# Performance work log

Measured on AMD Instinct MI355X. Metric: run time of the kernel, lower is better.

The kernel has to match this reference:

```python
import jax, jax.numpy as jnp
import numpy as np

N, C, E = 50000, 128, 600000


def setup_inputs() -> dict:
    key = jax.random.key(0)
    ks = jax.random.split(key, 10)
    s = 1.0 / np.sqrt(C)
    x = jax.random.normal(ks[0], (N, C), jnp.float32)
    edge_index = jax.random.randint(ks[1], (2, E), 0, N)
    edge_weight = jax.random.uniform(ks[2], (E,), jnp.float32)
    # learned params
    p_score = jax.random.normal(ks[3], (C,), jnp.float32) * s      # TopKPooling projection
    W0 = jax.random.normal(ks[4], (C, C), jnp.float32) * s         # initial GCN weight
    w_ih = jax.random.normal(ks[5], (3 * C, C), jnp.float32) * s   # GRU input weights (r,z,n)
    w_hh = jax.random.normal(ks[6], (3 * C, C), jnp.float32) * s   # GRU hidden weights
    b_ih = jnp.zeros((3 * C,), jnp.float32)
    b_hh = jnp.zeros((3 * C,), jnp.float32)
    w_lin = jax.random.normal(ks[7], (1, C), jnp.float32) * s      # head Linear(C,1)
    b_lin = jnp.zeros((1,), jnp.float32)
    return dict(x=x, edge_index=edge_index, edge_weight=edge_weight,
                p_score=p_score, W0=W0, w_ih=w_ih, w_hh=w_hh,
                b_ih=b_ih, b_hh=b_hh, w_lin=w_lin, b_lin=b_lin)


def _evolve_gcnh(x, edge_index, edge_weight, p_score, W0, w_ih, w_hh, b_ih, b_hh):
    n, c = x.shape
    # --- TopKPooling: score = tanh((x.p)/||p||), keep top k=C nodes, scale by score
    score = jnp.tanh((x @ p_score) / jnp.linalg.norm(p_score))
    vals, perm = jax.lax.top_k(score, c)           # tanh monotone -> same perm as raw score
    x_tilde = x[perm] * vals[:, None]              # [C, C]
    # --- GRU single step: batch = C rows of the weight matrix, hidden = W0
    gi = x_tilde @ w_ih.T + b_ih                   # [C, 3C]
    gh = W0 @ w_hh.T + b_hh                        # [C, 3C]
    i_r, i_z, i_n = jnp.split(gi, 3, axis=1)
    h_r, h_z, h_n = jnp.split(gh, 3, axis=1)
    r = jax.nn.sigmoid(i_r + h_r)
    z = jax.nn.sigmoid(i_z + h_z)
    ng = jnp.tanh(i_n + r * h_n)
    W = (1.0 - z) * ng + z * W0                    # evolved GCN weight [C, C]
    # --- GCNConv with fixed W: gcn_norm with self loops, then scatter-sum
    loops = jnp.arange(n)
    row = jnp.concatenate([edge_index[0], loops])  # source
    col = jnp.concatenate([edge_index[1], loops])  # target
    w = jnp.concatenate([edge_weight, jnp.ones((n,), edge_weight.dtype)])
    deg = jax.ops.segment_sum(w, col, num_segments=n)
    dis = jnp.where(deg > 0, jax.lax.rsqrt(jnp.where(deg > 0, deg, 1.0)), 0.0)
    norm = dis[row] * w * dis[col]                 # [E+N]
    xw = x @ W                                     # [N, C]
    out = jax.ops.segment_sum(norm[:, None] * xw[row], col, num_segments=n)
    return out


def reference(x, edge_index, edge_weight, p_score, W0, w_ih, w_hh, b_ih, b_hh, w_lin, b_lin):
    h = _evolve_gcnh(x, edge_index, edge_weight, p_score, W0, w_ih, w_hh, b_ih, b_hh)
    h = jax.nn.relu(h)
    return h @ w_lin.T + b_lin                     # [N, 1]
```

## Files before the change

### kernel.cpp

```cpp
#include <hip/hip_runtime.h>
#include <stdint.h>

#define C 128
#define RSTRIDE 64

typedef __attribute__((ext_vector_type(8))) short short8;
typedef __attribute__((ext_vector_type(4))) float f32x4;

__device__ __forceinline__ unsigned f32_orderable(float f) {
  unsigned u = __float_as_uint(f);
  return (u & 0x80000000u) ? ~u : (u | 0x80000000u);
}
__device__ __forceinline__ unsigned short f32_to_bf16_rn(float f) {
  unsigned u = __float_as_uint(f);
  unsigned rounding = 0x7FFFu + ((u >> 16) & 1u);
  return (unsigned short)((u + rounding) >> 16);
}
__device__ __forceinline__ float bf16_to_f32(unsigned short h) {
  return __uint_as_float(((unsigned)h) << 16);
}

__global__ __launch_bounds__(256) void k_score(const float* __restrict__ x,
                                               const float* __restrict__ p,
                                               float* __restrict__ score,
                                               unsigned* __restrict__ hist, int N) {
  int l = threadIdx.x & 63;
  int n = blockIdx.x * 4 + (threadIdx.x >> 6);
  if (n >= N) return;
  float2 xv = ((const float2*)(x + (size_t)n * C))[l];
  float2 pv = ((const float2*)p)[l];
  float s = xv.x * pv.x + xv.y * pv.y;
  for (int o = 32; o > 0; o >>= 1) s += __shfl_down(s, o, 64);
  if (l == 0) {
    score[n] = s;
    atomicAdd(&hist[f32_orderable(s) >> 16], 1u);
  }
}

__global__ __launch_bounds__(256) void k_fill(const int* __restrict__ ei,
                                              const float* __restrict__ ew,
                                              int* __restrict__ cnt,
                                              unsigned* __restrict__ csr, int E) {
  int base = (blockIdx.x * 256 + threadIdx.x) * 4;
  if (base >= E) return;
  if (base + 3 < E) {
    int4   s4 = *(const int4*)(ei + base);
    int4   d4 = *(const int4*)(ei + E + base);
    float4 w4 = *(const float4*)(ew + base);
    int r0 = atomicAdd(&cnt[d4.x], 1);
    int r1 = atomicAdd(&cnt[d4.y], 1);
    int r2 = atomicAdd(&cnt[d4.z], 1);
    int r3 = atomicAdd(&cnt[d4.w], 1);
    if (r0 > RSTRIDE - 1) r0 = RSTRIDE - 1;
    if (r1 > RSTRIDE - 1) r1 = RSTRIDE - 1;
    if (r2 > RSTRIDE - 1) r2 = RSTRIDE - 1;
    if (r3 > RSTRIDE - 1) r3 = RSTRIDE - 1;
    csr[((size_t)d4.x << 6) + r0] = ((unsigned)f32_to_bf16_rn(w4.x) << 16) | (unsigned)s4.x;
    csr[((size_t)d4.y << 6) + r1] = ((unsigned)f32_to_bf16_rn(w4.y) << 16) | (unsigned)s4.y;
    csr[((size_t)d4.z << 6) + r2] = ((unsigned)f32_to_bf16_rn(w4.z) << 16) | (unsigned)s4.z;
    csr[((size_t)d4.w << 6) + r3] = ((unsigned)f32_to_bf16_rn(w4.w) << 16) | (unsigned)s4.w;
  } else {
    for (int e = base; e < E; ++e) {
      int src = ei[e];
      int dst = ei[E + e];
      int r = atomicAdd(&cnt[dst], 1);
      if (r > RSTRIDE - 1) r = RSTRIDE - 1;
      csr[((size_t)dst << 6) + r] = ((unsigned)f32_to_bf16_rn(ew[e]) << 16) | (unsigned)src;
    }
  }
}

__global__ __launch_bounds__(1024) void k_topk_rowdeg(const unsigned* __restrict__ hist,
                                                      const float* __restrict__ score,
                                                      const float* __restrict__ p,
                                                      int* __restrict__ perm,
                                                      float* __restrict__ vals, int N,
                                                      const unsigned* __restrict__ csr,
                                                      const int* __restrict__ cnt,
                                                      float* __restrict__ dis) {
  int t = threadIdx.x;
  if (blockIdx.x == 0) {
    __shared__ unsigned csum[1024];
    __shared__ uint64_t keys[1024];
    __shared__ int tcs;
    __shared__ unsigned Ts, cnt_sh;
    __shared__ float s_inv;
    if (t < 64) {
      float2 v = ((const float2*)p)[t];
      float s = v.x * v.x + v.y * v.y;
      for (int o = 32; o > 0; o >>= 1) s += __shfl_down(s, o, 64);
      if (t == 0) s_inv = 1.0f / sqrtf(s);
    }
    if (t == 0) cnt_sh = 0;
    unsigned s = 0;
    const unsigned* hb = hist + t * 64;
    for (int b = 0; b < 64; ++b) s += hb[b];
    csum[t] = s;
    __syncthreads();
    for (int off = 1; off < 1024; off <<= 1) {
      unsigned v = (t + off < 1024) ? csum[t + off] : 0u;
      __syncthreads();
      csum[t] += v;
      __syncthreads();
    }
    unsigned St  = csum[t];
    unsigned St1 = (t < 1023) ? csum[t + 1] : 0u;
    if (St >= 128u && St1 < 128u) tcs = t;
    __syncthreads();
    if (t == 0) {
      int tc = tcs;
      unsigned cum = (tc < 1023) ? csum[tc + 1] : 0u;
      unsigned T = (unsigned)(tc * 64);
      for (int b = tc * 64 + 63; b >= tc * 64; --b) {
        cum += hist[b];
        if (cum >= 128u) { T = (unsigned)b; break; }
      }
      Ts = T;
    }
    __syncthreads();
    unsigned T = Ts;
    for (int k = t; k < N; k += 1024) {
      unsigned u = f32_orderable(score[k]);
      if ((u >> 16) >= T) {
        unsigned pos = atomicAdd(&cnt_sh, 1u);
        if (pos < 1024u) keys[pos] = ((uint64_t)u << 32) | (unsigned)(~k);
      }
    }
    __syncthreads();
    unsigned M = cnt_sh;
    if (M > 1024u) M = 1024u;
    if (t >= (int)M) keys[t] = 0ull;
    __syncthreads();
    for (int size = 2; size <= 1024; size <<= 1) {
      for (int stride = size >> 1; stride > 0; stride >>= 1) {
        int pr = t ^ stride;
        if (pr > t) {
          uint64_t a = keys[t], b = keys[pr];
          bool desc = ((t & size) == 0);
          if (desc ? (a < b) : (a > b)) { keys[t] = b; keys[pr] = a; }
        }
        __syncthreads();
      }
    }
    if (t < C) {
      uint64_t key = keys[t];
      unsigned n = ~(unsigned)(key & 0xFFFFFFFFull);
      unsigned u = (unsigned)(key >> 32);
      unsigned bbits = (u & 0x80000000u) ? (u & 0x7FFFFFFFu) : ~u;
      float sc = __uint_as_float(bbits);
      perm[t] = (int)n;
      vals[t] = tanhf(sc * s_inv);
    }
  } else {
    int n = (blockIdx.x - 1) * 128 + (t >> 3);
    if (n >= N) return;
    int l = t & 7;
    int c = cnt[n];
    if (c > RSTRIDE) c = RSTRIDE;
    const unsigned* row = csr + ((size_t)n << 6);
    float s = 0.0f;
    for (int i = l; i < c; i += 8) s += bf16_to_f32((unsigned short)(row[i] >> 16));
    for (int o = 4; o > 0; o >>= 1) s += __shfl_down(s, o, 8);
    if (l == 0) dis[n] = rsqrtf(1.0f + s);
  }
}

__global__ __launch_bounds__(128) void k_gru(const float* __restrict__ x,
                                             const int* __restrict__ perm,
                                             const float* __restrict__ vals,
                                             const float* __restrict__ W0,
                                             const float* __restrict__ w_ih,
                                             const float* __restrict__ w_hh,
                                             const float* __restrict__ b_ih,
                                             const float* __restrict__ b_hh,
                                             float* __restrict__ W) {
  __shared__ float xt[C], h0[C];
  int i = blockIdx.x, j = threadIdx.x;
  xt[j] = x[(size_t)perm[i] * C + j] * vals[i];
  h0[j] = W0[i * C + j];
  __syncthreads();
  float ir = b_ih[j], iz = b_ih[C + j], in_ = b_ih[2 * C + j];
  float hr = b_hh[j], hz = b_hh[C + j], hn  = b_hh[2 * C + j];
  const float4* wr = (const float4*)(w_ih + (size_t)j * C);
  const float4* wz = (const float4*)(w_ih + (size_t)(C + j) * C);
  const float4* wn = (const float4*)(w_ih + (size_t)(2 * C + j) * C);
  const float4* vr = (const float4*)(w_hh + (size_t)j * C);
  const float4* vz = (const float4*)(w_hh + (size_t)(C + j) * C);
  const float4* vn = (const float4*)(w_hh + (size_t)(2 * C + j) * C);
  const float4* xt4 = (const float4*)xt;
  const float4* h04 = (const float4*)h0;
  for (int k = 0; k < C / 4; ++k) {
    float4 xv = xt4[k], hv = h04[k], a;
    a = wr[k]; ir  += xv.x * a.x + xv.y * a.y + xv.z * a.z + xv.w * a.w;
    a = wz[k]; iz  += xv.x * a.x + xv.y * a.y + xv.z * a.z + xv.w * a.w;
    a = wn[k]; in_ += xv.x * a.x + xv.y * a.y + xv.z * a.z + xv.w * a.w;
    a = vr[k]; hr  += hv.x * a.x + hv.y * a.y + hv.z * a.z + hv.w * a.w;
    a = vz[k]; hz  += hv.x * a.x + hv.y * a.y + hv.z * a.z + hv.w * a.w;
    a = vn[k]; hn  += hv.x * a.x + hv.y * a.y + hv.z * a.z + hv.w * a.w;
  }
  float r  = 1.0f / (1.0f + expf(-(ir + hr)));
  float z  = 1.0f / (1.0f + expf(-(iz + hz)));
  float ng = tanhf(in_ + r * hn);
  W[i * C + j] = (1.0f - z) * ng + z * h0[j];
}

__global__ __launch_bounds__(256) void k_wsplit(const float* __restrict__ W,
                                                unsigned short* __restrict__ Bhi,
                                                unsigned short* __restrict__ Blo) {
  int gtid = blockIdx.x * 256 + threadIdx.x;
  int tile = gtid >> 6;
  int l = gtid & 63;
  int ct = tile >> 2, kt = tile & 3;
  int j = ct * 16 + (l & 15);
  int kbase = kt * 32 + (l >> 4) * 8;
  size_t o = (size_t)(tile * 64 + l) * 8;
#pragma unroll
  for (int e = 0; e < 8; ++e) {
    float w = W[(size_t)(kbase + e) * C + j];
    unsigned short hi = f32_to_bf16_rn(w);
    float rem = w - bf16_to_f32(hi);
    Bhi[o + e] = hi;
    Blo[o + e] = f32_to_bf16_rn(rem);
  }
}

__global__ __launch_bounds__(256) void k_xw(const float* __restrict__ x,
                                            const unsigned short* __restrict__ Bhi,
                                            const unsigned short* __restrict__ Blo,
                                            unsigned short* __restrict__ xwh, int N) {
  int wid = threadIdx.x >> 6;
  int l = threadIdx.x & 63;
  int rt = blockIdx.x * 4 + wid;
  int r0 = rt * 16;
  if (r0 >= N) return;
  int row16 = l & 15;
  int kgrp = l >> 4;

  short8 ahi[4], alo[4];
#pragma unroll
  for (int kt = 0; kt < 4; ++kt) {
    int r = r0 + row16;
    if (r >= N) r = N - 1;
    const float* xp = x + (size_t)r * C + kt * 32 + kgrp * 8;
    float4 a0 = *(const float4*)xp;
    float4 a1 = *(const float4*)(xp + 4);
    float v[8] = {a0.x, a0.y, a0.z, a0.w, a1.x, a1.y, a1.z, a1.w};
#pragma unroll
    for (int e = 0; e < 8; ++e) {
      unsigned short hi = f32_to_bf16_rn(v[e]);
      float rem = v[e] - bf16_to_f32(hi);
      ahi[kt][e] = (short)hi;
      alo[kt][e] = (short)f32_to_bf16_rn(rem);
    }
  }

  f32x4 acc[8];
#pragma unroll
  for (int ct = 0; ct < 8; ++ct) acc[ct] = (f32x4){0.f, 0.f, 0.f, 0.f};

#pragma unroll
  for (int ct = 0; ct < 8; ++ct) {
#pragma unroll
    for (int kt = 0; kt < 4; ++kt) {
      const short8 bhi = *(const short8*)(Bhi + (size_t)((ct * 4 + kt) * 64 + l) * 8);
      const short8 blo = *(const short8*)(Blo + (size_t)((ct * 4 + kt) * 64 + l) * 8);
      acc[ct] = __builtin_amdgcn_mfma_f32_16x16x32_bf16(ahi[kt], bhi, acc[ct], 0, 0, 0);
      acc[ct] = __builtin_amdgcn_mfma_f32_16x16x32_bf16(alo[kt], bhi, acc[ct], 0, 0, 0);
      acc[ct] = __builtin_amdgcn_mfma_f32_16x16x32_bf16(ahi[kt], blo, acc[ct], 0, 0, 0);
      acc[ct] = __builtin_amdgcn_mfma_f32_16x16x32_bf16(alo[kt], blo, acc[ct], 0, 0, 0);
    }
  }

#pragma unroll
  for (int ct = 0; ct < 8; ++ct) {
    int col = ct * 16 + row16;
#pragma unroll
    for (int reg = 0; reg < 4; ++reg) {
      int row = r0 + kgrp * 4 + reg;
      if (row < N) xwh[(size_t)row * C + col] = f32_to_bf16_rn(acc[ct][reg]);
    }
  }
}

__device__ __forceinline__ float4 bf16x4_to_f32(uint2 pk) {
  float4 r;
  r.x = __uint_as_float(pk.x << 16);
  r.y = __uint_as_float(pk.x & 0xFFFF0000u);
  r.z = __uint_as_float(pk.y << 16);
  r.w = __uint_as_float(pk.y & 0xFFFF0000u);
  return r;
}
__global__ __launch_bounds__(256) void k_gather_final(const unsigned* __restrict__ csr,
                                                      const int* __restrict__ cnt,
                                                      const unsigned short* __restrict__ xwh,
                                                      const float* __restrict__ dis,
                                                      const float* __restrict__ w_lin,
                                                      const float* __restrict__ b_lin,
                                                      float* __restrict__ out, int N) {
  int tid = threadIdx.x;
  int n = blockIdx.x * 8 + (tid >> 5);
  if (n >= N) return;
  int l = tid & 31;
  const unsigned* row = csr + ((size_t)n << 6);
  int c = cnt[n];
  if (c > RSTRIDE) c = RSTRIDE;
  float4 acc = make_float4(0.f, 0.f, 0.f, 0.f);

  unsigned ent[16];
#pragma unroll
  for (int i = 0; i < 16; ++i) ent[i] = row[i];
#pragma unroll
  for (int i = 0; i < 16; ++i) {
    int si = ent[i] & 0xFFFF;
    float wi = (i < c) ? bf16_to_f32((unsigned short)(ent[i] >> 16)) * dis[si] : 0.0f;
    uint2 pk = ((const uint2*)(xwh + (size_t)si * C))[l];
    float4 v = bf16x4_to_f32(pk);
    acc.x += wi * v.x;
    acc.y += wi * v.y;
    acc.z += wi * v.z;
    acc.w += wi * v.w;
  }
  for (int i = 16; i < c; ++i) {
    unsigned e0 = row[i];
    int s0 = e0 & 0xFFFF;
    float w0 = bf16_to_f32((unsigned short)(e0 >> 16)) * dis[s0];
    uint2 pk = ((const uint2*)(xwh + (size_t)s0 * C))[l];
    float4 v = bf16x4_to_f32(pk);
    acc.x += w0 * v.x;
    acc.y += w0 * v.y;
    acc.z += w0 * v.z;
    acc.w += w0 * v.w;
  }
  float dn = dis[n];
  uint2 ps = ((const uint2*)(xwh + (size_t)n * C))[l];
  float4 xv = bf16x4_to_f32(ps);
  acc.x = fmaf(dn, xv.x, acc.x) * dn;
  acc.y = fmaf(dn, xv.y, acc.y) * dn;
  acc.z = fmaf(dn, xv.z, acc.z) * dn;
  acc.w = fmaf(dn, xv.w, acc.w) * dn;
  float4 wl = ((const float4*)w_lin)[l];
  float psum = fmaxf(acc.x, 0.f) * wl.x + fmaxf(acc.y, 0.f) * wl.y
             + fmaxf(acc.z, 0.f) * wl.z + fmaxf(acc.w, 0.f) * wl.w;
  for (int o = 16; o > 0; o >>= 1) psum += __shfl_down(psum, o, 32);
  if (l == 0) out[n] = psum + b_lin[0];
}

extern "C" void kernel_launch(void* const* d_in, const int* in_sizes, int n_in,
                              void* d_out, int out_size, void* d_ws, size_t ws_size,
                              hipStream_t stream) {
  const float* x     = (const float*)d_in[0];
  const int*   ei    = (const int*)d_in[1];
  const float* ew    = (const float*)d_in[2];
  const float* p     = (const float*)d_in[3];
  const float* W0    = (const float*)d_in[4];
  const float* w_ih  = (const float*)d_in[5];
  const float* w_hh  = (const float*)d_in[6];
  const float* b_ih  = (const float*)d_in[7];
  const float* b_hh  = (const float*)d_in[8];
  const float* w_lin = (const float*)d_in[9];
  const float* b_lin = (const float*)d_in[10];
  int N = in_sizes[0] / C;
  int E = in_sizes[2];

  char* ws = (char*)d_ws;
  size_t off = 0;
  auto alloc = [&](size_t bytes) -> void* {
    void* q = ws + off;
    off = (off + bytes + 255) & ~(size_t)255;
    return q;
  };
  unsigned short* xwh = (unsigned short*)alloc((size_t)N * C * 2);
  unsigned* csr    = (unsigned*)alloc((size_t)N * RSTRIDE * 4);
  float*    score  = (float*)alloc((size_t)N * 4);
  float*    dis    = (float*)alloc((size_t)N * 4);
  size_t zstart = off;
  unsigned* hist   = (unsigned*)alloc(65536 * 4);
  int*      cnt    = (int*)alloc((size_t)N * 4);
  size_t zend = off;
  int*      perm   = (int*)alloc(C * 4);
  float*    vals   = (float*)alloc(C * 4);
  float*    W      = (float*)alloc(C * C * 4);
  unsigned short* Bhi = (unsigned short*)alloc(C * C * 2);
  unsigned short* Blo = (unsigned short*)alloc(C * C * 2);

  hipMemsetAsync(ws + zstart, 0, zend - zstart, stream);

  k_score<<<(N + 3) / 4, 256, 0, stream>>>(x, p, score, hist, N);
  k_fill<<<(E / 4 + 255) / 256, 256, 0, stream>>>(ei, ew, cnt, csr, E);
  int RB = (N + 127) / 128;
  k_topk_rowdeg<<<1 + RB, 1024, 0, stream>>>(hist, score, p, perm, vals, N, csr, cnt, dis);
  k_gru<<<C, C, 0, stream>>>(x, perm, vals, W0, w_ih, w_hh, b_ih, b_hh, W);
  k_wsplit<<<8, 256, 0, stream>>>(W, Bhi, Blo);
  {
    int rowtiles = (N + 15) / 16;
    int blocks = (rowtiles + 3) / 4;
    k_xw<<<blocks, 256, 0, stream>>>(x, Bhi, Blo, xwh, N);
  }
  k_gather_final<<<(N + 7) / 8, 256, 0, stream>>>(csr, cnt, xwh, dis,
                                                  w_lin, b_lin, (float*)d_out, N);
}
```

Measured before the change: 265.0 us.

## Fuse whole pipeline into one cooperative persistent kernel with grid syncs

Replaces the sequence of seven launches plus a memset with a single cooperative kernel that zeroes buffers, scores, builds the CSR, does top-k, runs the GRU, computes x@W with MFMA and gathers, separated by grid.sync barriers. It also folds the weight split into the GRU epilogue and overlaps the top-k selection (block 0) with the edge fill on the other blocks. This targets launch overhead and idle gaps between small kernels, at the cost of fewer resident blocks per phase (grid capped at 2048), a heavily serialized single-block top-k, and grid-wide barrier costs. A fallback multi-kernel path remains if the cooperative launch fails.

```diff
diff --git a/kernel.cpp b/kernel.cpp
--- a/kernel.cpp
+++ b/kernel.cpp
@@ -1,8 +1,12 @@
 #include <hip/hip_runtime.h>
+#include <hip/hip_cooperative_groups.h>
 #include <stdint.h>
+
+namespace cg = cooperative_groups;
 
 #define C 128
 #define RSTRIDE 64
+#define TPB 256
 
 typedef __attribute__((ext_vector_type(8))) short short8;
 typedef __attribute__((ext_vector_type(4))) float f32x4;
@@ -18,6 +22,323 @@
 }
 __device__ __forceinline__ float bf16_to_f32(unsigned short h) {
   return __uint_as_float(((unsigned)h) << 16);
+}
+__device__ __forceinline__ float4 bf16x4_to_f32(uint2 pk) {
+  float4 r;
+  r.x = __uint_as_float(pk.x << 16);
+  r.y = __uint_as_float(pk.x & 0xFFFF0000u);
+  r.z = __uint_as_float(pk.y << 16);
+  r.w = __uint_as_float(pk.y & 0xFFFF0000u);
+  return r;
+}
+
+__global__ __launch_bounds__(TPB) void k_mega(
+    const float* __restrict__ x, const float* __restrict__ p,
+    const int* __restrict__ ei, const float* __restrict__ ew,
+    const float* __restrict__ W0, const float* __restrict__ w_ih,
+    const float* __restrict__ w_hh, const float* __restrict__ b_ih,
+    const float* __restrict__ b_hh, const float* __restrict__ w_lin,
+    const float* __restrict__ b_lin,
+    float* __restrict__ score, unsigned* __restrict__ hist,
+    int* __restrict__ cnt, unsigned* __restrict__ csr,
+    float* __restrict__ dis, int* __restrict__ perm, float* __restrict__ vals,
+    unsigned short* __restrict__ Bhi, unsigned short* __restrict__ Blo,
+    unsigned short* __restrict__ xwh, float* __restrict__ out,
+    int N, int E) {
+  cg::grid_group grid = cg::this_grid();
+  const int b = blockIdx.x, t = threadIdx.x, G = gridDim.x;
+
+  __shared__ uint64_t keys[1024];
+  __shared__ unsigned csum[256];
+  __shared__ float sh_xt[2][C], sh_h0[2][C];
+  __shared__ int tcs;
+  __shared__ unsigned Ts, cnt_sh;
+  __shared__ float s_inv;
+
+  {
+    int ztot = 65536 + N;
+    for (int i = b * TPB + t; i < ztot; i += G * TPB) {
+      if (i < 65536) hist[i] = 0u; else cnt[i - 65536] = 0;
+    }
+  }
+  grid.sync();
+
+  {
+    int l = t & 63, w = t >> 6;
+    for (int base = b * 4; base < N; base += G * 4) {
+      int n = base + w;
+      if (n < N) {
+        float2 xv = ((const float2*)(x + (size_t)n * C))[l];
+        float2 pv = ((const float2*)p)[l];
+        float s = xv.x * pv.x + xv.y * pv.y;
+        for (int o = 32; o > 0; o >>= 1) s += __shfl_down(s, o, 64);
+        if (l == 0) {
+          score[n] = s;
+          atomicAdd(&hist[f32_orderable(s) >> 16], 1u);
+        }
+      }
+    }
+  }
+  grid.sync();
+
+  if (b == 0) {
+    if (t < 64) {
+      float2 v = ((const float2*)p)[t];
+      float s = v.x * v.x + v.y * v.y;
+      for (int o = 32; o > 0; o >>= 1) s += __shfl_down(s, o, 64);
+      if (t == 0) s_inv = 1.0f / sqrtf(s);
+    }
+    if (t == 0) cnt_sh = 0u;
+    unsigned s = 0;
+    const unsigned* hb = hist + t * 256;
+    for (int i = 0; i < 256; ++i) s += hb[i];
+    csum[t] = s;
+    __syncthreads();
+    for (int off = 1; off < 256; off <<= 1) {
+      unsigned v = (t + off < 256) ? csum[t + off] : 0u;
+      __syncthreads();
+      csum[t] += v;
+      __syncthreads();
+    }
+    unsigned St  = csum[t];
+    unsigned St1 = (t < 255) ? csum[t + 1] : 0u;
+    if (St >= 128u && St1 < 128u) tcs = t;
+    __syncthreads();
+    if (t == 0) {
+      int tc = tcs;
+      unsigned cum = (tc < 255) ? csum[tc + 1] : 0u;
+      unsigned T = (unsigned)(tc * 256);
+      for (int fb = tc * 256 + 255; fb >= tc * 256; --fb) {
+        cum += hist[fb];
+        if (cum >= 128u) { T = (unsigned)fb; break; }
+      }
+      Ts = T;
+    }
+    __syncthreads();
+    unsigned T = Ts;
+    for (int k = t; k < N; k += TPB) {
+      unsigned u = f32_orderable(score[k]);
+      if ((u >> 16) >= T) {
+        unsigned pos = atomicAdd(&cnt_sh, 1u);
+        if (pos < 1024u) keys[pos] = ((uint64_t)u << 32) | (unsigned)(~k);
+      }
+    }
+    __syncthreads();
+    unsigned M = cnt_sh;
+    if (M > 1024u) M = 1024u;
+    for (int i = t; i < 1024; i += TPB) if (i >= (int)M) keys[i] = 0ull;
+    __syncthreads();
+    for (int size = 2; size <= 1024; size <<= 1) {
+      for (int stride = size >> 1; stride > 0; stride >>= 1) {
+        for (int q = t; q < 512; q += TPB) {
+          int i = 2 * q - (q & (stride - 1));
+          int j = i + stride;
+          uint64_t a = keys[i], bb = keys[j];
+          bool desc = ((i & size) == 0);
+          if (desc ? (a < bb) : (a > bb)) { keys[i] = bb; keys[j] = a; }
+        }
+        __syncthreads();
+      }
+    }
+    if (t < C) {
+      uint64_t key = keys[t];
+      unsigned n = ~(unsigned)(key & 0xFFFFFFFFull);
+      unsigned u = (unsigned)(key >> 32);
+      unsigned bbits = (u & 0x80000000u) ? (u & 0x7FFFFFFFu) : ~u;
+      perm[t] = (int)n;
+      vals[t] = tanhf(__uint_as_float(bbits) * s_inv);
+    }
+  } else {
+    int items = (E + 3) >> 2;
+    for (int i = (b - 1) * TPB + t; i < items; i += (G - 1) * TPB) {
+      int base = i * 4;
+      if (base + 3 < E) {
+        int4   s4 = *(const int4*)(ei + base);
+        int4   d4 = *(const int4*)(ei + E + base);
+        float4 w4 = *(const float4*)(ew + base);
+        int r0 = atomicAdd(&cnt[d4.x], 1);
+        int r1 = atomicAdd(&cnt[d4.y], 1);
+        int r2 = atomicAdd(&cnt[d4.z], 1);
+        int r3 = atomicAdd(&cnt[d4.w], 1);
+        r0 = min(r0, RSTRIDE - 1);
+        r1 = min(r1, RSTRIDE - 1);
+        r2 = min(r2, RSTRIDE - 1);
+        r3 = min(r3, RSTRIDE - 1);
+        csr[((size_t)d4.x << 6) + r0] = ((unsigned)f32_to_bf16_rn(w4.x) << 16) | (unsigned)s4.x;
+        csr[((size_t)d4.y << 6) + r1] = ((unsigned)f32_to_bf16_rn(w4.y) << 16) | (unsigned)s4.y;
+        csr[((size_t)d4.z << 6) + r2] = ((unsigned)f32_to_bf16_rn(w4.z) << 16) | (unsigned)s4.z;
+        csr[((size_t)d4.w << 6) + r3] = ((unsigned)f32_to_bf16_rn(w4.w) << 16) | (unsigned)s4.w;
+      } else {
+        for (int e = base; e < E; ++e) {
+          int src = ei[e];
+          int dst = ei[E + e];
+          int r = min(atomicAdd(&cnt[dst], 1), RSTRIDE - 1);
+          csr[((size_t)dst << 6) + r] = ((unsigned)f32_to_bf16_rn(ew[e]) << 16) | (unsigned)src;
+        }
+      }
+    }
+  }
+  grid.sync();
+
+  if (b < 64) {
+    int half = t >> 7, j = t & 127;
+    int ri = b * 2 + half;
+    sh_xt[half][j] = x[(size_t)perm[ri] * C + j] * vals[ri];
+    sh_h0[half][j] = W0[ri * C + j];
+    __syncthreads();
+    float ir = b_ih[j], iz = b_ih[C + j], in_ = b_ih[2 * C + j];
+    float hr = b_hh[j], hz = b_hh[C + j], hn  = b_hh[2 * C + j];
+    const float4* wr = (const float4*)(w_ih + (size_t)j * C);
+    const float4* wz = (const float4*)(w_ih + (size_t)(C + j) * C);
+    const float4* wn = (const float4*)(w_ih + (size_t)(2 * C + j) * C);
+    const float4* vr = (const float4*)(w_hh + (size_t)j * C);
+    const float4* vz = (const float4*)(w_hh + (size_t)(C + j) * C);
+    const float4* vn = (const float4*)(w_hh + (size_t)(2 * C + j) * C);
+    const float4* xt4 = (const float4*)sh_xt[half];
+    const float4* h04 = (const float4*)sh_h0[half];
+    for (int k = 0; k < C / 4; ++k) {
+      float4 xv = xt4[k], hv = h04[k], a;
+      a = wr[k]; ir  += xv.x * a.x + xv.y * a.y + xv.z * a.z + xv.w * a.w;
+      a = wz[k]; iz  += xv.x * a.x + xv.y * a.y + xv.z * a.z + xv.w * a.w;
+      a = wn[k]; in_ += xv.x * a.x + xv.y * a.y + xv.z * a.z + xv.w * a.w;
+      a = vr[k]; hr  += hv.x * a.x + hv.y * a.y + hv.z * a.z + hv.w * a.w;
+      a = vz[k]; hz  += hv.x * a.x + hv.y * a.y + hv.z * a.z + hv.w * a.w;
+      a = vn[k]; hn  += hv.x * a.x + hv.y * a.y + hv.z * a.z + hv.w * a.w;
+    }
+    float r  = 1.0f / (1.0f + expf(-(ir + hr)));
+    float z  = 1.0f / (1.0f + expf(-(iz + hz)));
+    float ng = tanhf(in_ + r * hn);
+    float w = (1.0f - z) * ng + z * sh_h0[half][j];
+    int ct = j >> 4, kt = ri >> 5;
+    int tile = ct * 4 + kt;
+    int l2 = (j & 15) | (((ri >> 3) & 3) << 4);
+    int e2 = ri & 7;
+    size_t o = ((size_t)(tile * 64 + l2)) * 8 + e2;
+    unsigned short hi = f32_to_bf16_rn(w);
+    float rem = w - bf16_to_f32(hi);
+    Bhi[o] = hi;
+    Blo[o] = f32_to_bf16_rn(rem);
+  } else {
+    int NBR = G - 64;
+    for (int base = (b - 64) * 32; base < N; base += NBR * 32) {
+      int n = base + (t >> 3);
+      if (n < N) {
+        int l = t & 7;
+        int c = cnt[n];
+        if (c > RSTRIDE) c = RSTRIDE;
+        const unsigned* row = csr + ((size_t)n << 6);
+        float s = 0.0f;
+        for (int i = l; i < c; i += 8) s += bf16_to_f32((unsigned short)(row[i] >> 16));
+        for (int o = 4; o > 0; o >>= 1) s += __shfl_down(s, o, 8);
+        if (l == 0) dis[n] = rsqrtf(1.0f + s);
+      }
+    }
+  }
+  grid.sync();
+
+  {
+    int wid = t >> 6, l = t & 63;
+    int row16 = l & 15, kgrp = l >> 4;
+    int RT = (N + 15) / 16;
+    for (int rt0 = b * 4; rt0 < RT; rt0 += G * 4) {
+      int rt = rt0 + wid;
+      int r0 = rt * 16;
+      if (r0 < N) {
+        short8 ahi[4], alo[4];
+#pragma unroll
+        for (int kt = 0; kt < 4; ++kt) {
+          int r = r0 + row16;
+          if (r >= N) r = N - 1;
+          const float* xp = x + (size_t)r * C + kt * 32 + kgrp * 8;
+          float4 a0 = *(const float4*)xp;
+          float4 a1 = *(const float4*)(xp + 4);
+          float v[8] = {a0.x, a0.y, a0.z, a0.w, a1.x, a1.y, a1.z, a1.w};
+#pragma unroll
+          for (int e = 0; e < 8; ++e) {
+            unsigned short hi = f32_to_bf16_rn(v[e]);
+            float rem = v[e] - bf16_to_f32(hi);
+            ahi[kt][e] = (short)hi;
+            alo[kt][e] = (short)f32_to_bf16_rn(rem);
+          }
+        }
+        f32x4 acc[8];
+#pragma unroll
+        for (int ct = 0; ct < 8; ++ct) acc[ct] = (f32x4){0.f, 0.f, 0.f, 0.f};
+#pragma unroll
+        for (int ct = 0; ct < 8; ++ct) {
+#pragma unroll
+          for (int kt = 0; kt < 4; ++kt) {
+            const short8 bhi = *(const short8*)(Bhi + (size_t)((ct * 4 + kt) * 64 + l) * 8);
+            const short8 blo = *(const short8*)(Blo + (size_t)((ct * 4 + kt) * 64 + l) * 8);
+            acc[ct] = __builtin_amdgcn_mfma_f32_16x16x32_bf16(ahi[kt], bhi, acc[ct], 0, 0, 0);
+            acc[ct] = __builtin_amdgcn_mfma_f32_16x16x32_bf16(alo[kt], bhi, acc[ct], 0, 0, 0);
+            acc[ct] = __builtin_amdgcn_mfma_f32_16x16x32_bf16(ahi[kt], blo, acc[ct], 0, 0, 0);
+            acc[ct] = __builtin_amdgcn_mfma_f32_16x16x32_bf16(alo[kt], blo, acc[ct], 0, 0, 0);
+          }
+        }
+#pragma unroll
+        for (int ct = 0; ct < 8; ++ct) {
+          int col = ct * 16 + row16;
+#pragma unroll
+          for (int reg = 0; reg < 4; ++reg) {
+            int row = r0 + kgrp * 4 + reg;
+            if (row < N) xwh[(size_t)row * C + col] = f32_to_bf16_rn(acc[ct][reg]);
+          }
+        }
+      }
+    }
+  }
+  grid.sync();
+
+  {
+    int l = t & 31;
+    for (int base = b * 8; base < N; base += G * 8) {
+      int n = base + (t >> 5);
+      if (n < N) {
+        const unsigned* row = csr + ((size_t)n << 6);
+        int c = cnt[n];
+        if (c > RSTRIDE) c = RSTRIDE;
+        float4 acc = make_float4(0.f, 0.f, 0.f, 0.f);
+        unsigned ent[16];
+#pragma unroll
+        for (int i = 0; i < 16; ++i) ent[i] = row[i];
+#pragma unroll
+        for (int i = 0; i < 16; ++i) {
+          int si = ent[i] & 0xFFFF;
+          float wi = (i < c) ? bf16_to_f32((unsigned short)(ent[i] >> 16)) * dis[si] : 0.0f;
+          uint2 pk = ((const uint2*)(xwh + (size_t)si * C))[l];
+          float4 v = bf16x4_to_f32(pk);
+          acc.x += wi * v.x;
+          acc.y += wi * v.y;
+          acc.z += wi * v.z;
+          acc.w += wi * v.w;
+        }
+        for (int i = 16; i < c; ++i) {
+          unsigned e0 = row[i];
+          int s0 = e0 & 0xFFFF;
+          float w0 = bf16_to_f32((unsigned short)(e0 >> 16)) * dis[s0];
+          uint2 pk = ((const uint2*)(xwh + (size_t)s0 * C))[l];
+          float4 v = bf16x4_to_f32(pk);
+          acc.x += w0 * v.x;
+          acc.y += w0 * v.y;
+          acc.z += w0 * v.z;
+          acc.w += w0 * v.w;
+        }
+        float dn = dis[n];
+        uint2 ps = ((const uint2*)(xwh + (size_t)n * C))[l];
+        float4 xv = bf16x4_to_f32(ps);
+        acc.x = fmaf(dn, xv.x, acc.x) * dn;
+        acc.y = fmaf(dn, xv.y, acc.y) * dn;
+        acc.z = fmaf(dn, xv.z, acc.z) * dn;
+        acc.w = fmaf(dn, xv.w, acc.w) * dn;
+        float4 wl = ((const float4*)w_lin)[l];
+        float psum = fmaxf(acc.x, 0.f) * wl.x + fmaxf(acc.y, 0.f) * wl.y
+                   + fmaxf(acc.z, 0.f) * wl.z + fmaxf(acc.w, 0.f) * wl.w;
+        for (int o = 16; o > 0; o >>= 1) psum += __shfl_down(psum, o, 32);
+        if (l == 0) out[n] = psum + b_lin[0];
+      }
+    }
+  }
 }
 
 __global__ __launch_bounds__(256) void k_score(const float* __restrict__ x,
@@ -51,10 +372,10 @@
     int r1 = atomicAdd(&cnt[d4.y], 1);
     int r2 = atomicAdd(&cnt[d4.z], 1);
     int r3 = atomicAdd(&cnt[d4.w], 1);
-    if (r0 > RSTRIDE - 1) r0 = RSTRIDE - 1;
-    if (r1 > RSTRIDE - 1) r1 = RSTRIDE - 1;
-    if (r2 > RSTRIDE - 1) r2 = RSTRIDE - 1;
-    if (r3 > RSTRIDE - 1) r3 = RSTRIDE - 1;
+    r0 = min(r0, RSTRIDE - 1);
+    r1 = min(r1, RSTRIDE - 1);
+    r2 = min(r2, RSTRIDE - 1);
+    r3 = min(r3, RSTRIDE - 1);
     csr[((size_t)d4.x << 6) + r0] = ((unsigned)f32_to_bf16_rn(w4.x) << 16) | (unsigned)s4.x;
     csr[((size_t)d4.y << 6) + r1] = ((unsigned)f32_to_bf16_rn(w4.y) << 16) | (unsigned)s4.y;
     csr[((size_t)d4.z << 6) + r2] = ((unsigned)f32_to_bf16_rn(w4.z) << 16) | (unsigned)s4.z;
@@ -63,8 +384,7 @@
     for (int e = base; e < E; ++e) {
       int src = ei[e];
       int dst = ei[E + e];
-      int r = atomicAdd(&cnt[dst], 1);
-      if (r > RSTRIDE - 1) r = RSTRIDE - 1;
+      int r = min(atomicAdd(&cnt[dst], 1), RSTRIDE - 1);
       csr[((size_t)dst << 6) + r] = ((unsigned)f32_to_bf16_rn(ew[e]) << 16) | (unsigned)src;
     }
   }
@@ -147,9 +467,8 @@
       unsigned n = ~(unsigned)(key & 0xFFFFFFFFull);
       unsigned u = (unsigned)(key >> 32);
       unsigned bbits = (u & 0x80000000u) ? (u & 0x7FFFFFFFu) : ~u;
-      float sc = __uint_as_float(bbits);
       perm[t] = (int)n;
-      vals[t] = tanhf(sc * s_inv);
+      vals[t] = tanhf(__uint_as_float(bbits) * s_inv);
     }
   } else {
     int n = (blockIdx.x - 1) * 128 + (t >> 3);
@@ -173,7 +492,8 @@
                                              const float* __restrict__ w_hh,
                                              const float* __restrict__ b_ih,
                                              const float* __restrict__ b_hh,
-                                             float* __restrict__ W) {
+                                             unsigned short* __restrict__ Bhi,
+                                             unsigned short* __restrict__ Blo) {
   __shared__ float xt[C], h0[C];
   int i = blockIdx.x, j = threadIdx.x;
   xt[j] = x[(size_t)perm[i] * C + j] * vals[i];
@@ -201,27 +521,16 @@
   float r  = 1.0f / (1.0f + expf(-(ir + hr)));
   float z  = 1.0f / (1.0f + expf(-(iz + hz)));
   float ng = tanhf(in_ + r * hn);
-  W[i * C + j] = (1.0f - z) * ng + z * h0[j];
-}
-
-__global__ __launch_bounds__(256) void k_wsplit(const float* __restrict__ W,
-                                                unsigned short* __restrict__ Bhi,
-                                                unsigned short* __restrict__ Blo) {
-  int gtid = blockIdx.x * 256 + threadIdx.x;
-  int tile = gtid >> 6;
-  int l = gtid & 63;
-  int ct = tile >> 2, kt = tile & 3;
-  int j = ct * 16 + (l & 15);
-  int kbase = kt * 32 + (l >> 4) * 8;
-  size_t o = (size_t)(tile * 64 + l) * 8;
-#pragma unroll
-  for (int e = 0; e < 8; ++e) {
-    float w = W[(size_t)(kbase + e) * C + j];
-    unsigned short hi = f32_to_bf16_rn(w);
-    float rem = w - bf16_to_f32(hi);
-    Bhi[o + e] = hi;
-    Blo[o + e] = f32_to_bf16_rn(rem);
-  }
+  float w = (1.0f - z) * ng + z * h0[j];
+  int ct = j >> 4, kt = i >> 5;
+  int tile = ct * 4 + kt;
+  int l2 = (j & 15) | (((i >> 3) & 3) << 4);
+  int e2 = i & 7;
+  size_t o = ((size_t)(tile * 64 + l2)) * 8 + e2;
+  unsigned short hi = f32_to_bf16_rn(w);
+  float rem = w - bf16_to_f32(hi);
+  Bhi[o] = hi;
+  Blo[o] = f32_to_bf16_rn(rem);
 }
 
 __global__ __launch_bounds__(256) void k_xw(const float* __restrict__ x,
@@ -235,7 +544,6 @@
   if (r0 >= N) return;
   int row16 = l & 15;
   int kgrp = l >> 4;
-
   short8 ahi[4], alo[4];
 #pragma unroll
   for (int kt = 0; kt < 4; ++kt) {
@@ -253,11 +561,9 @@
       alo[kt][e] = (short)f32_to_bf16_rn(rem);
     }
   }
-
   f32x4 acc[8];
 #pragma unroll
   for (int ct = 0; ct < 8; ++ct) acc[ct] = (f32x4){0.f, 0.f, 0.f, 0.f};
-
 #pragma unroll
   for (int ct = 0; ct < 8; ++ct) {
 #pragma unroll
@@ -270,7 +576,6 @@
       acc[ct] = __builtin_amdgcn_mfma_f32_16x16x32_bf16(alo[kt], blo, acc[ct], 0, 0, 0);
     }
   }
-
 #pragma unroll
   for (int ct = 0; ct < 8; ++ct) {
     int col = ct * 16 + row16;
@@ -282,14 +587,6 @@
   }
 }
 
-__device__ __forceinline__ float4 bf16x4_to_f32(uint2 pk) {
-  float4 r;
-  r.x = __uint_as_float(pk.x << 16);
-  r.y = __uint_as_float(pk.x & 0xFFFF0000u);
-  r.z = __uint_as_float(pk.y << 16);
-  r.w = __uint_as_float(pk.y & 0xFFFF0000u);
-  return r;
-}
 __global__ __launch_bounds__(256) void k_gather_final(const unsigned* __restrict__ csr,
                                                       const int* __restrict__ cnt,
                                                       const unsigned short* __restrict__ xwh,
@@ -305,7 +602,6 @@
   int c = cnt[n];
   if (c > RSTRIDE) c = RSTRIDE;
   float4 acc = make_float4(0.f, 0.f, 0.f, 0.f);
-
   unsigned ent[16];
 #pragma unroll
   for (int i = 0; i < 16; ++i) ent[i] = row[i];
@@ -359,6 +655,7 @@
   const float* b_hh  = (const float*)d_in[8];
   const float* w_lin = (const float*)d_in[9];
   const float* b_lin = (const float*)d_in[10];
+  float* outp = (float*)d_out;
   int N = in_sizes[0] / C;
   int E = in_sizes[2];
 
@@ -373,29 +670,40 @@
   unsigned* csr    = (unsigned*)alloc((size_t)N * RSTRIDE * 4);
   float*    score  = (float*)alloc((size_t)N * 4);
   float*    dis    = (float*)alloc((size_t)N * 4);
-  size_t zstart = off;
   unsigned* hist   = (unsigned*)alloc(65536 * 4);
   int*      cnt    = (int*)alloc((size_t)N * 4);
-  size_t zend = off;
   int*      perm   = (int*)alloc(C * 4);
   float*    vals   = (float*)alloc(C * 4);
-  float*    W      = (float*)alloc(C * C * 4);
   unsigned short* Bhi = (unsigned short*)alloc(C * C * 2);
   unsigned short* Blo = (unsigned short*)alloc(C * C * 2);
 
-  hipMemsetAsync(ws + zstart, 0, zend - zstart, stream);
-
-  k_score<<<(N + 3) / 4, 256, 0, stream>>>(x, p, score, hist, N);
-  k_fill<<<(E / 4 + 255) / 256, 256, 0, stream>>>(ei, ew, cnt, csr, E);
-  int RB = (N + 127) / 128;
-  k_topk_rowdeg<<<1 + RB, 1024, 0, stream>>>(hist, score, p, perm, vals, N, csr, cnt, dis);
-  k_gru<<<C, C, 0, stream>>>(x, perm, vals, W0, w_ih, w_hh, b_ih, b_hh, W);
-  k_wsplit<<<8, 256, 0, stream>>>(W, Bhi, Blo);
-  {
+  int nb = 0;
+  hipError_t qerr = hipOccupancyMaxActiveBlocksPerMultiprocessor(&nb, k_mega, TPB, 0);
+  int G = (qerr == hipSuccess && nb > 0) ? nb * 256 : 512;
+  if (G > 2048) G = 2048;
+  if (G < 128) G = 128;
+
+  void* args[] = {(void*)&x, (void*)&p, (void*)&ei, (void*)&ew, (void*)&W0,
+                  (void*)&w_ih, (void*)&w_hh, (void*)&b_ih, (void*)&b_hh,
+                  (void*)&w_lin, (void*)&b_lin,
+                  (void*)&score, (void*)&hist, (void*)&cnt, (void*)&csr,
+                  (void*)&dis, (void*)&perm, (void*)&vals,
+                  (void*)&Bhi, (void*)&Blo, (void*)&xwh, (void*)&outp,
+                  (void*)&N, (void*)&E};
+  hipError_t err = hipLaunchCooperativeKernel(k_mega, dim3(G), dim3(TPB),
+                                              args, 0, stream);
+  if (err != hipSuccess) {
+    char zbuf = 0; (void)zbuf;
+    hipMemsetAsync(hist, 0, 65536 * 4, stream);
+    hipMemsetAsync(cnt, 0, (size_t)N * 4, stream);
+    k_score<<<(N + 3) / 4, 256, 0, stream>>>(x, p, score, hist, N);
+    k_fill<<<(E / 4 + 255) / 256, 256, 0, stream>>>(ei, ew, cnt, csr, E);
+    int RB = (N + 127) / 128;
+    k_topk_rowdeg<<<1 + RB, 1024, 0, stream>>>(hist, score, p, perm, vals, N, csr, cnt, dis);
+    k_gru<<<C, C, 0, stream>>>(x, perm, vals, W0, w_ih, w_hh, b_ih, b_hh, Bhi, Blo);
     int rowtiles = (N + 15) / 16;
-    int blocks = (rowtiles + 3) / 4;
-    k_xw<<<blocks, 256, 0, stream>>>(x, Bhi, Blo, xwh, N);
-  }
-  k_gather_final<<<(N + 7) / 8, 256, 0, stream>>>(csr, cnt, xwh, dis,
-                                                  w_lin, b_lin, (float*)d_out, N);
-}
+    k_xw<<<(rowtiles + 3) / 4, 256, 0, stream>>>(x, Bhi, Blo, xwh, N);
+    k_gather_final<<<(N + 7) / 8, 256, 0, stream>>>(csr, cnt, xwh, dis,
+                                                    w_lin, b_lin, outp, N);
+  }
+}
```

Result: slower. 589.3 us (+122.4%).
